# Optimization experiments

Hardware: AMD Instinct MI355X
Metric: run time of the kernel (lower is better)

Reference implementation:

```python
import jax, jax.numpy as jnp
import numpy as np

BATCH = 8      # pairing batch_size from __init__
NUM_POS = 4    # instances per identity
HEAD = 8
T = 50.0       # softmax temperature
FDIM = 2048
H, W = 24, 12
N = BATCH * NUM_POS          # samples per modality (32)
D = FDIM // HEAD             # per-head feature dim (256)
S = H * W                    # spatial positions (288)


def _pairs(rng, offset):
    # mirrors CM_Attention._random_pairs
    pos = np.concatenate([rng.permutation(NUM_POS) + NUM_POS * b for b in range(BATCH)])
    neg = []
    for b in range(BATCH):
        others = np.array([x for x in range(BATCH) if x != b])
        bidx = rng.choice(others, NUM_POS, replace=False)
        nidx = rng.permutation(NUM_POS)
        neg.append(bidx * NUM_POS + nidx)
    return pos + offset, np.concatenate(neg) + offset


def setup_inputs() -> dict:
    key = jax.random.key(0)
    kv, kt = jax.random.split(key)
    feat_v = jax.random.normal(kv, (N, FDIM, H, W), jnp.float32)
    feat_t = jax.random.normal(kt, (N, FDIM, H, W), jnp.float32)
    rng = np.random.default_rng(0)
    pos_v, neg_v = _pairs(rng, 0)
    pos_t, neg_t = _pairs(rng, N)   # text indices offset by batch_size*num_pos
    pos_idx = jnp.asarray(np.concatenate([pos_v, pos_t]), jnp.int32)
    neg_idx = jnp.asarray(np.concatenate([neg_v, neg_t]), jnp.int32)
    return {"feat_v": feat_v, "feat_t": feat_t, "pos_idx": pos_idx, "neg_idx": neg_idx}


def _k_x_q(fq, fk):
    # fq, fk: [B, H, D, h, w] -> row-softmax of temperature-scaled cosine sim [B,H,S,S]
    B, Hh, Dd, h, w = fq.shape
    q = fq.reshape(B, Hh, Dd, h * w).transpose(0, 1, 3, 2)  # [B,H,S,D]
    k = fk.reshape(B, Hh, Dd, h * w).transpose(0, 1, 3, 2)
    qn = q / jnp.maximum(jnp.linalg.norm(q, axis=-1, keepdims=True), 1e-12)
    kn = k / jnp.maximum(jnp.linalg.norm(k, axis=-1, keepdims=True), 1e-12)
    sim = jnp.einsum('bhsd,bhtd->bhst', qn, kn)
    # exp(t*(sim-max))/sum == softmax(t*sim)
    return jax.nn.softmax(T * sim, axis=-1)


def _warp(KQ, fk):
    # KQ: [B,H,S,S], fk: [B,H,D,h,w] -> warped features [B,H,D,h,w]
    B, Hh, Dd, h, w = fk.shape
    k = fk.reshape(B, Hh, Dd, h * w)
    out = jnp.einsum('bhst,bhdt->bhds', KQ, k)
    return out.reshape(B, Hh, Dd, h, w)


def _mask(feat):
    # per-head spatial L2 norm, min-max normalized -> [B,H,1,h,w] (detached)
    B, Hh, Dd, h, w = feat.shape
    n = jnp.linalg.norm(feat, axis=2).reshape(B, Hh, h * w)
    n = n - n.min(axis=-1, keepdims=True)
    n = n / (n.max(axis=-1, keepdims=True) + 1e-12)
    return jax.lax.stop_gradient(n.reshape(B, Hh, 1, h, w))


def _comask(KQ, mq, mk):
    # mq, mk: [B,H,1,h,w] -> co-attention mask [B,1,h,w] (detached)
    B, Hh, _, h, w = mq.shape
    q = mq.reshape(B, Hh, 1, h * w).transpose(0, 1, 3, 2)  # [B,H,S,1]
    k = mk.reshape(B, Hh, 1, h * w).transpose(0, 1, 3, 2)
    c = (q * (KQ @ k)).reshape(B, Hh, h * w)
    c = jnp.linalg.norm(c, axis=1)                          # norm over heads -> [B,S]
    c = c - c.min(axis=-1, keepdims=True)
    c = c / (c.max(axis=-1, keepdims=True) + 1e-12)
    return jax.lax.stop_gradient(c.reshape(B, 1, h, w))


def reference(feat_v, feat_t, pos_idx, neg_idx):
    feat = jnp.concatenate([feat_v, feat_t], axis=0)        # [2N, FDIM, H, W]
    B = feat.shape[0]
    fmh = feat.reshape(B, HEAD, D, H, W)
    fpos = feat[pos_idx].reshape(B, HEAD, D, H, W)
    fneg = feat[neg_idx].reshape(B, HEAD, D, H, W)

    mask = _mask(fmh)
    KQp = _k_x_q(fmh, fpos)
    comask_pos = _comask(KQp, mask, mask[pos_idx])
    recon_pos = (mask * _warp(KQp, fpos) + (1.0 - mask) * fmh).reshape(B, FDIM, H, W)

    KQn = _k_x_q(fmh, fneg)
    recon_neg = (mask * _warp(KQn, fneg) + (1.0 - mask) * fmh).reshape(B, FDIM, H, W)

    # TripletMarginLoss(margin=0.3, p=2, reduction='none') with pairwise L2
    # distance along the channel dim (dim=1) -> per-location loss [B, H, W]
    eps = 1e-6
    d_ap = jnp.linalg.norm(feat - recon_pos + eps, axis=1)
    d_an = jnp.linalg.norm(feat - recon_neg + eps, axis=1)
    trip = jnp.maximum(d_ap - d_an + 0.3, 0.0)
    # comask_pos [B,1,H,W] * trip [B,H,W] broadcasts (as in torch) to [B,B,H,W]
    loss = jnp.mean(comask_pos * trip)
    return recon_pos, loss
```

## Files before the change

kernel.cpp:

```cpp
#include <hip/hip_runtime.h>
#include <math.h>

#define NB 64
#define NH 8
#define ND 256
#define NS 288
#define NF 2048
#define HALF_N 32

#define RECON_ELEMS ((size_t)NB * NF * NS)

#define WS_NORM   0
#define WS_MASK   (NB*NH*NS)
#define WS_CPOS   (2*NB*NH*NS)
#define WS_COMASK (3*NB*NH*NS)
#define WS_AP     (3*NB*NH*NS + NB*NS)
#define WS_AN     (4*NB*NH*NS + NB*NS)
#define WS_PROD   (5*NB*NH*NS + NB*NS)

typedef short bf16x8 __attribute__((ext_vector_type(8)));
typedef short bf16x4 __attribute__((ext_vector_type(4)));
typedef float f32x4  __attribute__((ext_vector_type(4)));

__device__ __forceinline__ unsigned short f2bf(float f) {
    unsigned int u = __float_as_uint(f);
    return (unsigned short)((u + 0x7fffu + ((u >> 16) & 1u)) >> 16);
}

__device__ __forceinline__ const float* feat_ptr(const float* fv, const float* ft, int b) {
    return (b < HALF_N) ? fv + (size_t)b * NF * NS : ft + (size_t)(b - HALF_N) * NF * NS;
}

__global__ __launch_bounds__(256) void norm_mask_kernel(
        const float* __restrict__ fv, const float* __restrict__ ft,
        float* __restrict__ normArr, float* __restrict__ maskArr) {
    const int bh = blockIdx.x;
    const int b = bh >> 3, h = bh & 7;
    const float* f = feat_ptr(fv, ft, b) + (size_t)h * ND * NS;
    const int tid = threadIdx.x;
    __shared__ float smn[256], smx[256];

    const int s1 = tid, s2 = tid + 256;
    float n1 = 0.f, n2 = 0.f;
    for (int d = 0; d < ND; ++d) {
        float v1 = f[d * NS + s1];
        n1 += v1 * v1;
        if (s2 < NS) { float v2 = f[d * NS + s2]; n2 += v2 * v2; }
    }
    n1 = sqrtf(n1);
    float lmn = n1, lmx = n1;
    if (s2 < NS) { n2 = sqrtf(n2); lmn = fminf(lmn, n2); lmx = fmaxf(lmx, n2); }
    normArr[bh * NS + s1] = n1;
    if (s2 < NS) normArr[bh * NS + s2] = n2;

    smn[tid] = lmn; smx[tid] = lmx;
    __syncthreads();
    for (int off = 128; off > 0; off >>= 1) {
        if (tid < off) {
            smn[tid] = fminf(smn[tid], smn[tid + off]);
            smx[tid] = fmaxf(smx[tid], smx[tid + off]);
        }
        __syncthreads();
    }
    const float mn = smn[0];
    const float inv = 1.0f / (smx[0] - mn + 1e-12f);
    maskArr[bh * NS + s1] = (n1 - mn) * inv;
    if (s2 < NS) maskArr[bh * NS + s2] = (n2 - mn) * inv;
}

#define DPT 264
#define TCP 36

__global__ __launch_bounds__(384, 2) void attn_kernel(
        const float* __restrict__ fv, const float* __restrict__ ft,
        const int* __restrict__ pos_idx, const int* __restrict__ neg_idx,
        const float* __restrict__ normArr, const float* __restrict__ maskArr,
        float* __restrict__ out_recon, float* __restrict__ c_pos,
        float* __restrict__ ap_part, float* __restrict__ an_part) {
    const int sblk = blockIdx.x;
    const int bh   = blockIdx.y;
    const int pass = blockIdx.z;
    const int b = bh >> 3, h = bh & 7;
    const int p = (pass == 0) ? pos_idx[b] : neg_idx[b];
    const float* fq = feat_ptr(fv, ft, b) + (size_t)h * ND * NS;
    const float* fk = feat_ptr(fv, ft, p) + (size_t)h * ND * NS;

    __shared__ __align__(16) unsigned short ldsKT[32 * DPT];
    __shared__ __align__(16) unsigned short ldsKN[256 * TCP];
    __shared__ float ldsRKN[NS];
    __shared__ float ldsMK[NS];

    const int tid = threadIdx.x;
    const int a   = tid & 15;
    const int g   = (tid >> 4) & 3;
    const int qt  = tid >> 6;
    const int sq  = sblk * 96 + qt * 16 + a;

    for (int i = tid; i < NS; i += 384) {
        ldsRKN[i] = 1.0f / fmaxf(normArr[(p * NH + h) * NS + i], 1e-12f);
        ldsMK[i]  = maskArr[(p * NH + h) * NS + i];
    }
    const float rq = 1.0f / fmaxf(normArr[bh * NS + sq], 1e-12f);
    const float mq = maskArr[bh * NS + sq];

    bf16x8 qf[8];
    #pragma unroll
    for (int ks = 0; ks < 8; ++ks) {
        #pragma unroll
        for (int j = 0; j < 8; ++j)
            qf[ks][j] = (short)f2bf(fq[(32 * ks + 8 * g + j) * NS + sq]);
    }

    f32x4 accO[16];
    #pragma unroll
    for (int i = 0; i < 16; ++i) accO[i] = (f32x4){0.f, 0.f, 0.f, 0.f};
    float lsum = 0.f, csum = 0.f;

    const int t2 = tid & 15;
    const int dg = tid >> 4;

    for (int tc = 0; tc < NS; tc += 32) {
        __syncthreads();
        for (int d = dg; d < 256; d += 24) {
            const float2 v = *(const float2*)&fk[d * NS + tc + 2 * t2];
            const unsigned int b0 = f2bf(v.x), b1 = f2bf(v.y);
            *(unsigned int*)&ldsKN[d * TCP + 2 * t2] = b0 | (b1 << 16);
            ldsKT[(2 * t2) * DPT + d]     = (unsigned short)b0;
            ldsKT[(2 * t2 + 1) * DPT + d] = (unsigned short)b1;
        }
        __syncthreads();

        f32x4 sacc0 = {0.f,0.f,0.f,0.f}, sacc1 = {0.f,0.f,0.f,0.f};
        #pragma unroll
        for (int ks = 0; ks < 8; ++ks) {
            const bf16x8 ka0 = *(const bf16x8*)&ldsKT[a * DPT + 32 * ks + 8 * g];
            const bf16x8 ka1 = *(const bf16x8*)&ldsKT[(a + 16) * DPT + 32 * ks + 8 * g];
            sacc0 = __builtin_amdgcn_mfma_f32_16x16x32_bf16(ka0, qf[ks], sacc0, 0, 0, 0);
            sacc1 = __builtin_amdgcn_mfma_f32_16x16x32_bf16(ka1, qf[ks], sacc1, 0, 0, 0);
        }

        bf16x8 pf;
        #pragma unroll
        for (int r = 0; r < 4; ++r) {
            const int t0 = tc + 4 * g + r;
            const float p0 = __expf(50.0f * sacc0[r] * rq * ldsRKN[t0]);
            lsum += p0; csum += p0 * ldsMK[t0];
            pf[r] = (short)f2bf(p0);
            const int t1 = tc + 16 + 4 * g + r;
            const float p1 = __expf(50.0f * sacc1[r] * rq * ldsRKN[t1]);
            lsum += p1; csum += p1 * ldsMK[t1];
            pf[4 + r] = (short)f2bf(p1);
        }

        #pragma unroll
        for (int dt = 0; dt < 16; ++dt) {
            const int row = dt * 16 + a;
            const bf16x4 lo = *(const bf16x4*)&ldsKN[row * TCP + 4 * g];
            const bf16x4 hi = *(const bf16x4*)&ldsKN[row * TCP + 16 + 4 * g];
            bf16x8 va;
            va[0]=lo[0]; va[1]=lo[1]; va[2]=lo[2]; va[3]=lo[3];
            va[4]=hi[0]; va[5]=hi[1]; va[6]=hi[2]; va[7]=hi[3];
            accO[dt] = __builtin_amdgcn_mfma_f32_16x16x32_bf16(va, pf, accO[dt], 0, 0, 0);
        }
    }

    lsum += __shfl_xor(lsum, 16); lsum += __shfl_xor(lsum, 32);
    csum += __shfl_xor(csum, 16); csum += __shfl_xor(csum, 32);
    const float linv = 1.0f / lsum;
    if (pass == 0 && (tid & 63) < 16)
        c_pos[bh * NS + sq] = mq * csum * linv;

    float ss = 0.f;
    #pragma unroll
    for (int dt = 0; dt < 16; ++dt) {
        #pragma unroll
        for (int r = 0; r < 4; ++r) {
            const int d = dt * 16 + 4 * g + r;
            const float o = accO[dt][r] * linv;
            const float f = fq[d * NS + sq];
            const float diff = mq * (f - o) + 1e-6f;
            ss += diff * diff;
            if (pass == 0)
                out_recon[((size_t)b * NF + (size_t)h * ND + d) * NS + sq] = f + mq * (o - f);
        }
    }
    ss += __shfl_xor(ss, 16); ss += __shfl_xor(ss, 32);
    if ((tid & 63) < 16) {
        float* dst = (pass == 0) ? ap_part : an_part;
        dst[bh * NS + sq] = ss;
    }
}

__global__ __launch_bounds__(256) void comask_kernel(
        const float* __restrict__ c_pos, float* __restrict__ comask) {
    const int b = blockIdx.x;
    const int tid = threadIdx.x;
    __shared__ float smn[256], smx[256];
    const int s1 = tid, s2 = tid + 256;
    float c1 = 0.f, c2 = 0.f;
    for (int h = 0; h < NH; ++h) {
        const float v = c_pos[(b * NH + h) * NS + s1];
        c1 += v * v;
        if (s2 < NS) { const float w = c_pos[(b * NH + h) * NS + s2]; c2 += w * w; }
    }
    c1 = sqrtf(c1);
    float lmn = c1, lmx = c1;
    if (s2 < NS) { c2 = sqrtf(c2); lmn = fminf(lmn, c2); lmx = fmaxf(lmx, c2); }
    smn[tid] = lmn; smx[tid] = lmx;
    __syncthreads();
    for (int off = 128; off > 0; off >>= 1) {
        if (tid < off) {
            smn[tid] = fminf(smn[tid], smn[tid + off]);
            smx[tid] = fmaxf(smx[tid], smx[tid + off]);
        }
        __syncthreads();
    }
    const float mn = smn[0];
    const float inv = 1.0f / (smx[0] - mn + 1e-12f);
    comask[b * NS + s1] = (c1 - mn) * inv;
    if (s2 < NS) comask[b * NS + s2] = (c2 - mn) * inv;
}

__global__ __launch_bounds__(64) void loss_partial(
        const float* __restrict__ comask, const float* __restrict__ ap_part,
        const float* __restrict__ an_part, float* __restrict__ prod) {
    const int s = blockIdx.x;
    const int bb = threadIdx.x;
    float sap = 0.f, san = 0.f;
    for (int hh = 0; hh < NH; ++hh) {
        sap += ap_part[(bb * NH + hh) * NS + s];
        san += an_part[(bb * NH + hh) * NS + s];
    }
    float trip = fmaxf(sqrtf(sap) - sqrtf(san) + 0.3f, 0.0f);
    float cm = comask[bb * NS + s];
    #pragma unroll
    for (int off = 32; off > 0; off >>= 1) {
        trip += __shfl_xor(trip, off);
        cm   += __shfl_xor(cm, off);
    }
    if (bb == 0) prod[s] = trip * cm;
}

__global__ __launch_bounds__(64) void loss_final(
        const float* __restrict__ prod, float* __restrict__ out_loss) {
    const int tid = threadIdx.x;
    float sum = 0.f;
    for (int i = tid; i < NS; i += 64) sum += prod[i];
    #pragma unroll
    for (int off = 32; off > 0; off >>= 1) sum += __shfl_xor(sum, off);
    if (tid == 0) out_loss[0] = sum * (1.0f / ((float)NB * (float)NB * (float)NS));
}

extern "C" void kernel_launch(void* const* d_in, const int* in_sizes, int n_in,
                              void* d_out, int out_size, void* d_ws, size_t ws_size,
                              hipStream_t stream) {
    const float* fv = (const float*)d_in[0];
    const float* ft = (const float*)d_in[1];
    const int* pos  = (const int*)d_in[2];
    const int* neg  = (const int*)d_in[3];
    float* out = (float*)d_out;
    float* ws  = (float*)d_ws;

    float* normArr = ws + WS_NORM;
    float* maskArr = ws + WS_MASK;
    float* c_pos   = ws + WS_CPOS;
    float* comask  = ws + WS_COMASK;
    float* ap      = ws + WS_AP;
    float* an      = ws + WS_AN;
    float* prod    = ws + WS_PROD;

    norm_mask_kernel<<<dim3(NB * NH), dim3(256), 0, stream>>>(fv, ft, normArr, maskArr);
    attn_kernel<<<dim3(3, NB * NH, 2), dim3(384), 0, stream>>>(
        fv, ft, pos, neg, normArr, maskArr, out, c_pos, ap, an);
    comask_kernel<<<dim3(NB), dim3(256), 0, stream>>>(c_pos, comask);
    loss_partial<<<dim3(NS), dim3(64), 0, stream>>>(comask, ap, an, prod);
    loss_final<<<dim3(1), dim3(64), 0, stream>>>(prod, out + RECON_ELEMS);
}
```

Measured before the change: 999.1 us.

## Precompute bf16 feature copies in both layouts and feed attention from them

A preprocessing pass now writes bf16 copies of all features into workspace in two layouts: d-major, fused into the norm/mask kernel, and s-major, via a new transpose kernel. A new attention kernel loads K and V tiles straight from these bf16 buffers with register-prefetched 16-byte loads, instead of converting fp32 inside every attention block. This targets the repeated fp32 reads and conversions done because each key feature is reused by several query blocks and both passes. It costs extra workspace and an additional conversion pass, and it falls back to the old path only when the workspace is too small.

```diff
diff --git a/kernel.cpp b/kernel.cpp
--- a/kernel.cpp
+++ b/kernel.cpp
@@ -17,6 +17,8 @@
 #define WS_AP     (3*NB*NH*NS + NB*NS)
 #define WS_AN     (4*NB*NH*NS + NB*NS)
 #define WS_PROD   (5*NB*NH*NS + NB*NS)
+#define WS_BF_OFF ((size_t)4 << 20)
+#define BF_ONE    ((size_t)NB * NH * NS * ND * 2)
 
 typedef short bf16x8 __attribute__((ext_vector_type(8)));
 typedef short bf16x4 __attribute__((ext_vector_type(4)));
@@ -30,6 +32,222 @@
 __device__ __forceinline__ const float* feat_ptr(const float* fv, const float* ft, int b) {
     return (b < HALF_N) ? fv + (size_t)b * NF * NS : ft + (size_t)(b - HALF_N) * NF * NS;
 }
+
+
+__global__ __launch_bounds__(256) void convKN_norm_mask(
+        const float* __restrict__ fv, const float* __restrict__ ft,
+        float* __restrict__ normArr, float* __restrict__ maskArr,
+        unsigned short* __restrict__ featKN) {
+    const int bh = blockIdx.x;
+    const int b = bh >> 3, h = bh & 7;
+    const float* f = feat_ptr(fv, ft, b) + (size_t)h * ND * NS;
+    unsigned short* kn = featKN + (size_t)bh * ND * NS;
+    const int tid = threadIdx.x;
+    __shared__ float smn[256], smx[256];
+
+    const int s1 = tid, s2 = tid + 256;
+    float n1 = 0.f, n2 = 0.f;
+    for (int d = 0; d < ND; ++d) {
+        float v1 = f[d * NS + s1];
+        n1 += v1 * v1;
+        kn[d * NS + s1] = f2bf(v1);
+        if (s2 < NS) {
+            float v2 = f[d * NS + s2];
+            n2 += v2 * v2;
+            kn[d * NS + s2] = f2bf(v2);
+        }
+    }
+    n1 = sqrtf(n1);
+    float lmn = n1, lmx = n1;
+    if (s2 < NS) { n2 = sqrtf(n2); lmn = fminf(lmn, n2); lmx = fmaxf(lmx, n2); }
+    normArr[bh * NS + s1] = n1;
+    if (s2 < NS) normArr[bh * NS + s2] = n2;
+
+    smn[tid] = lmn; smx[tid] = lmx;
+    __syncthreads();
+    for (int off = 128; off > 0; off >>= 1) {
+        if (tid < off) {
+            smn[tid] = fminf(smn[tid], smn[tid + off]);
+            smx[tid] = fmaxf(smx[tid], smx[tid + off]);
+        }
+        __syncthreads();
+    }
+    const float mn = smn[0];
+    const float inv = 1.0f / (smx[0] - mn + 1e-12f);
+    maskArr[bh * NS + s1] = (n1 - mn) * inv;
+    if (s2 < NS) maskArr[bh * NS + s2] = (n2 - mn) * inv;
+}
+
+__global__ __launch_bounds__(256) void convKT(
+        const float* __restrict__ fv, const float* __restrict__ ft,
+        unsigned short* __restrict__ featKT) {
+    const int s0 = blockIdx.x * 32;
+    const int bh = blockIdx.y;
+    const int b = bh >> 3, h = bh & 7;
+    const float* f = feat_ptr(fv, ft, b) + (size_t)h * ND * NS;
+    const int tid = threadIdx.x;
+    __shared__ unsigned short tile[256 * 33];
+
+    const int sc = tid & 31;
+    for (int d = tid >> 5; d < ND; d += 8)
+        tile[d * 33 + sc] = f2bf(f[(size_t)d * NS + s0 + sc]);
+    __syncthreads();
+
+    for (int u = tid; u < 1024; u += 256) {
+        const int s_r = u >> 5;
+        const int du  = u & 31;
+        bf16x8 v;
+        #pragma unroll
+        for (int j = 0; j < 8; ++j) v[j] = tile[(du * 8 + j) * 33 + s_r];
+        *(bf16x8*)&featKT[((size_t)bh * NS + s0 + s_r) * ND + du * 8] = v;
+    }
+}
+
+#define DPT 264
+#define TCP 36
+
+__global__ __launch_bounds__(384, 2) void attn_fast(
+        const unsigned short* __restrict__ featKT,
+        const unsigned short* __restrict__ featKN,
+        const float* __restrict__ fv, const float* __restrict__ ft,
+        const int* __restrict__ pos_idx, const int* __restrict__ neg_idx,
+        const float* __restrict__ normArr, const float* __restrict__ maskArr,
+        float* __restrict__ out_recon, float* __restrict__ c_pos,
+        float* __restrict__ ap_part, float* __restrict__ an_part) {
+    const int sblk = blockIdx.x;
+    const int bh   = blockIdx.y;
+    const int pass = blockIdx.z;
+    const int b = bh >> 3, h = bh & 7;
+    const int p = (pass == 0) ? pos_idx[b] : neg_idx[b];
+    const int bhk = p * NH + h;
+    const float* fq = feat_ptr(fv, ft, b) + (size_t)h * ND * NS;
+
+    __shared__ __align__(16) unsigned short ldsKT[32 * DPT];
+    __shared__ __align__(16) unsigned short ldsKN[256 * TCP];
+    __shared__ float ldsRKN[NS];
+    __shared__ float ldsMK[NS];
+
+    const int tid = threadIdx.x;
+    const int a   = tid & 15;
+    const int g   = (tid >> 4) & 3;
+    const int qt  = tid >> 6;
+    const int sq  = sblk * 96 + qt * 16 + a;
+
+    for (int i = tid; i < NS; i += 384) {
+        ldsRKN[i] = 1.0f / fmaxf(normArr[bhk * NS + i], 1e-12f);
+        ldsMK[i]  = maskArr[bhk * NS + i];
+    }
+    const float rq = 1.0f / fmaxf(normArr[bh * NS + sq], 1e-12f);
+    const float mq = maskArr[bh * NS + sq];
+
+    bf16x8 qf[8];
+    {
+        const unsigned short* qrow = featKT + ((size_t)bh * NS + sq) * ND;
+        #pragma unroll
+        for (int ks = 0; ks < 8; ++ks)
+            qf[ks] = *(const bf16x8*)&qrow[32 * ks + 8 * g];
+    }
+
+    f32x4 accO[16];
+    #pragma unroll
+    for (int i = 0; i < 16; ++i) accO[i] = (f32x4){0.f, 0.f, 0.f, 0.f};
+    float lsum = 0.f, csum = 0.f;
+
+    const unsigned short* kT = featKT + (size_t)bhk * NS * ND;
+    const unsigned short* kN = featKN + (size_t)bhk * ND * NS;
+
+    bf16x8 rT[3], rN[3];
+    #define ISSUE(tc_) {                                                        \
+        _Pragma("unroll")                                                       \
+        for (int k = 0; k < 3; ++k) {                                           \
+            const int i = tid + 384 * k;                                        \
+            if (i < 1024) {                                                     \
+                rT[k] = *(const bf16x8*)&kT[(size_t)((tc_) + (i >> 5)) * ND + (i & 31) * 8]; \
+                rN[k] = *(const bf16x8*)&kN[(size_t)(i >> 2) * NS + (tc_) + (i & 3) * 8];    \
+            }                                                                   \
+        }                                                                       \
+    }
+
+    ISSUE(0);
+    for (int tc = 0; tc < NS; tc += 32) {
+        __syncthreads();
+        #pragma unroll
+        for (int k = 0; k < 3; ++k) {
+            const int i = tid + 384 * k;
+            if (i < 1024) {
+                *(bf16x8*)&ldsKT[(i >> 5) * DPT + (i & 31) * 8] = rT[k];
+                bf16x4 lo, hi;
+                lo[0]=rN[k][0]; lo[1]=rN[k][1]; lo[2]=rN[k][2]; lo[3]=rN[k][3];
+                hi[0]=rN[k][4]; hi[1]=rN[k][5]; hi[2]=rN[k][6]; hi[3]=rN[k][7];
+                *(bf16x4*)&ldsKN[(i >> 2) * TCP + (i & 3) * 8]     = lo;
+                *(bf16x4*)&ldsKN[(i >> 2) * TCP + (i & 3) * 8 + 4] = hi;
+            }
+        }
+        if (tc + 32 < NS) ISSUE(tc + 32);
+        __syncthreads();
+
+        f32x4 sacc0 = {0.f,0.f,0.f,0.f}, sacc1 = {0.f,0.f,0.f,0.f};
+        #pragma unroll
+        for (int ks = 0; ks < 8; ++ks) {
+            const bf16x8 ka0 = *(const bf16x8*)&ldsKT[a * DPT + 32 * ks + 8 * g];
+            const bf16x8 ka1 = *(const bf16x8*)&ldsKT[(a + 16) * DPT + 32 * ks + 8 * g];
+            sacc0 = __builtin_amdgcn_mfma_f32_16x16x32_bf16(ka0, qf[ks], sacc0, 0, 0, 0);
+            sacc1 = __builtin_amdgcn_mfma_f32_16x16x32_bf16(ka1, qf[ks], sacc1, 0, 0, 0);
+        }
+
+        bf16x8 pf;
+        #pragma unroll
+        for (int r = 0; r < 4; ++r) {
+            const int t0 = tc + 4 * g + r;
+            const float p0 = __expf(50.0f * sacc0[r] * rq * ldsRKN[t0]);
+            lsum += p0; csum += p0 * ldsMK[t0];
+            pf[r] = (short)f2bf(p0);
+            const int t1 = tc + 16 + 4 * g + r;
+            const float p1 = __expf(50.0f * sacc1[r] * rq * ldsRKN[t1]);
+            lsum += p1; csum += p1 * ldsMK[t1];
+            pf[4 + r] = (short)f2bf(p1);
+        }
+
+        #pragma unroll
+        for (int dt = 0; dt < 16; ++dt) {
+            const int row = dt * 16 + a;
+            const bf16x4 lo = *(const bf16x4*)&ldsKN[row * TCP + 4 * g];
+            const bf16x4 hi = *(const bf16x4*)&ldsKN[row * TCP + 16 + 4 * g];
+            bf16x8 va;
+            va[0]=lo[0]; va[1]=lo[1]; va[2]=lo[2]; va[3]=lo[3];
+            va[4]=hi[0]; va[5]=hi[1]; va[6]=hi[2]; va[7]=hi[3];
+            accO[dt] = __builtin_amdgcn_mfma_f32_16x16x32_bf16(va, pf, accO[dt], 0, 0, 0);
+        }
+    }
+    #undef ISSUE
+
+    lsum += __shfl_xor(lsum, 16); lsum += __shfl_xor(lsum, 32);
+    csum += __shfl_xor(csum, 16); csum += __shfl_xor(csum, 32);
+    const float linv = 1.0f / lsum;
+    if (pass == 0 && (tid & 63) < 16)
+        c_pos[bh * NS + sq] = mq * csum * linv;
+
+    float ss = 0.f;
+    #pragma unroll
+    for (int dt = 0; dt < 16; ++dt) {
+        #pragma unroll
+        for (int r = 0; r < 4; ++r) {
+            const int d = dt * 16 + 4 * g + r;
+            const float o = accO[dt][r] * linv;
+            const float f = fq[d * NS + sq];
+            const float diff = mq * (f - o) + 1e-6f;
+            ss += diff * diff;
+            if (pass == 0)
+                out_recon[((size_t)b * NF + (size_t)h * ND + d) * NS + sq] = f + mq * (o - f);
+        }
+    }
+    ss += __shfl_xor(ss, 16); ss += __shfl_xor(ss, 32);
+    if ((tid & 63) < 16) {
+        float* dst = (pass == 0) ? ap_part : an_part;
+        dst[bh * NS + sq] = ss;
+    }
+}
+
 
 __global__ __launch_bounds__(256) void norm_mask_kernel(
         const float* __restrict__ fv, const float* __restrict__ ft,
@@ -67,9 +285,6 @@
     maskArr[bh * NS + s1] = (n1 - mn) * inv;
     if (s2 < NS) maskArr[bh * NS + s2] = (n2 - mn) * inv;
 }
-
-#define DPT 264
-#define TCP 36
 
 __global__ __launch_bounds__(384, 2) void attn_kernel(
         const float* __restrict__ fv, const float* __restrict__ ft,
@@ -191,6 +406,7 @@
     }
 }
 
+
 __global__ __launch_bounds__(256) void comask_kernel(
         const float* __restrict__ c_pos, float* __restrict__ comask) {
     const int b = blockIdx.x;
@@ -269,9 +485,19 @@
     float* an      = ws + WS_AN;
     float* prod    = ws + WS_PROD;
 
-    norm_mask_kernel<<<dim3(NB * NH), dim3(256), 0, stream>>>(fv, ft, normArr, maskArr);
-    attn_kernel<<<dim3(3, NB * NH, 2), dim3(384), 0, stream>>>(
-        fv, ft, pos, neg, normArr, maskArr, out, c_pos, ap, an);
+    const size_t need = WS_BF_OFF + 2 * BF_ONE;
+    if (ws_size >= need) {
+        unsigned short* featKT = (unsigned short*)((char*)d_ws + WS_BF_OFF);
+        unsigned short* featKN = (unsigned short*)((char*)d_ws + WS_BF_OFF + BF_ONE);
+        convKN_norm_mask<<<dim3(NB * NH), dim3(256), 0, stream>>>(fv, ft, normArr, maskArr, featKN);
+        convKT<<<dim3(9, NB * NH), dim3(256), 0, stream>>>(fv, ft, featKT);
+        attn_fast<<<dim3(3, NB * NH, 2), dim3(384), 0, stream>>>(
+            featKT, featKN, fv, ft, pos, neg, normArr, maskArr, out, c_pos, ap, an);
+    } else {
+        norm_mask_kernel<<<dim3(NB * NH), dim3(256), 0, stream>>>(fv, ft, normArr, maskArr);
+        attn_kernel<<<dim3(3, NB * NH, 2), dim3(384), 0, stream>>>(
+            fv, ft, pos, neg, normArr, maskArr, out, c_pos, ap, an);
+    }
     comask_kernel<<<dim3(NB), dim3(256), 0, stream>>>(c_pos, comask);
     loss_partial<<<dim3(NS), dim3(64), 0, stream>>>(comask, ap, an, prod);
     loss_final<<<dim3(1), dim3(64), 0, stream>>>(prod, out + RECON_ELEMS);
```

After: 876.6 us. 12.3% less time.
